# Kernel tuning notes

Hardware: AMD Instinct MI355X
Metric: run time of the kernel (lower is better)

The kernel has to match this reference:

```python
import jax, jax.numpy as jnp
import numpy as np

B, L, D, H, K_DELAYS = 8, 2048, 512, 8, 8
DH = D // H


def setup_inputs() -> dict:
    key = jax.random.key(0)
    ks = jax.random.split(key, 6)
    def lin_w(k):
        return 0.02 * jax.random.normal(k, (D, D), jnp.float32)
    return {
        "x_q":  jax.random.normal(ks[0], (B, L, D), jnp.float32),
        "x_kv": jax.random.normal(ks[1], (B, L, D), jnp.float32),
        "Wq": lin_w(ks[2]), "bq": jnp.zeros((D,), jnp.float32),
        "Wk": lin_w(ks[3]), "bk": jnp.zeros((D,), jnp.float32),
        "Wv": lin_w(ks[4]), "bv": jnp.zeros((D,), jnp.float32),
        "Wo": lin_w(ks[5]), "bo": jnp.zeros((D,), jnp.float32),
    }


def reference(x_q, x_kv, Wq, bq, Wk, bk, Wv, bv, Wo, bo):
    Bx, Lx, Dx = x_q.shape

    def proj(x, W, b):  # torch Linear: x @ W.T + b, then split heads -> [B,H,L,dh]
        return (x @ W.T + b).reshape(Bx, Lx, H, DH).transpose(0, 2, 1, 3)

    q = proj(x_q, Wq, bq)
    k = proj(x_kv, Wk, bk)
    v = proj(x_kv, Wv, bv)

    # FFT-based autocorrelation over the time axis (axis=2)
    qz = q - q.mean(axis=2, keepdims=True)
    kz = k - k.mean(axis=2, keepdims=True)
    Qf = jnp.fft.rfft(qz, axis=2)
    Kf = jnp.fft.rfft(kz, axis=2)
    corr = jnp.fft.irfft(Qf * jnp.conj(Kf), n=Lx, axis=2).mean(axis=-1)  # [B,H,L]
    # torch expands corr to [B,H,Lq,Lk] then means over Lq -> identical to corr
    score = corr

    K = min(K_DELAYS, Lx)
    vals, idx = jax.lax.top_k(score, K)                    # [B,H,K]
    w = vals / (vals.sum(axis=-1, keepdims=True) + 1e-12)
    w = jax.lax.stop_gradient(w)                           # .detach() in torch

    # circular shift by -delay == gather at (t + delay) mod L
    t = jnp.arange(Lx)
    pos = (t[None, None, None, :] + idx[..., None]) % Lx   # [B,H,K,L]
    v_sh = jnp.take_along_axis(v[:, :, None, :, :], pos[..., None], axis=3)  # [B,H,K,L,dh]
    out = jnp.einsum('bhk,bhkld->bhld', w, v_sh)           # weighted sum over delays

    out = out.transpose(0, 2, 1, 3).reshape(Bx, Lx, Dx)
    return out @ Wo.T + bo
```

## Files before the change

### kernel.cpp

```cpp
#include <hip/hip_runtime.h>
#include <math.h>

#define BB 8
#define LL 2048
#define DD 512
#define HH 8
#define DHH 64
#define KD 8
#define MM (BB*LL)

typedef _Float16 f16x2 __attribute__((ext_vector_type(2)));
typedef _Float16 f16x4 __attribute__((ext_vector_type(4)));
typedef _Float16 f16x8 __attribute__((ext_vector_type(8)));
typedef float    f32x4 __attribute__((ext_vector_type(4)));

__device__ inline void cvt8(const float* __restrict__ s, _Float16* hp, _Float16* lp) {
    const float4 a = *(const float4*)s;
    const float4 b = *(const float4*)(s + 4);
    const float v[8] = {a.x, a.y, a.z, a.w, b.x, b.y, b.z, b.w};
    f16x8 hi, lo;
#pragma unroll
    for (int j = 0; j < 8; j++) {
        const _Float16 h = (_Float16)v[j];
        hi[j] = h;
        lo[j] = (_Float16)((v[j] - (float)h) * 512.0f);
    }
    *(f16x8*)hp = hi;
    if (lp) *(f16x8*)lp = lo;
}

__global__ __launch_bounds__(256) void prep_all(const float* __restrict__ xq,
                                                const float* __restrict__ xkv,
                                                const float* __restrict__ Wq, const float* __restrict__ Wk,
                                                const float* __restrict__ Wv, const float* __restrict__ Wo,
                                                _Float16* __restrict__ Xq_h, _Float16* __restrict__ Xq_l,
                                                _Float16* __restrict__ Xkv_h, _Float16* __restrict__ Xkv_l,
                                                _Float16* __restrict__ Wq_h, _Float16* __restrict__ Wq_l,
                                                _Float16* __restrict__ Wk_h, _Float16* __restrict__ Wk_l,
                                                _Float16* __restrict__ Wv_h, _Float16* __restrict__ Wo_h) {
    const int bid = blockIdx.x;
    if (bid < 8192) {
        const int g = bid * 256 + threadIdx.x;
        const int which = g >> 20;
        const size_t idx = (size_t)(g & 1048575) * 8;
        const float* src = which ? xkv : xq;
        _Float16* dh = which ? Xkv_h : Xq_h;
        _Float16* dl = which ? Xkv_l : Xq_l;
        cvt8(src + idx, dh + idx, dl + idx);
    } else {
        const int g = (bid - 8192) * 256 + threadIdx.x;
        const int which = g >> 15;
        const size_t idx = (size_t)(g & 32767) * 8;
        if (which == 0)      cvt8(Wq + idx, Wq_h + idx, Wq_l + idx);
        else if (which == 1) cvt8(Wk + idx, Wk_h + idx, Wk_l + idx);
        else if (which == 2) cvt8(Wv + idx, Wv_h + idx, nullptr);
        else                 cvt8(Wo + idx, Wo_h + idx, nullptr);
    }
}

template<int NPROD, int MODE>
__device__ __forceinline__ void gemm_body(const _Float16* __restrict__ Ag,
                                          const _Float16* __restrict__ Al_g,
                                          const _Float16* __restrict__ Bg,
                                          const _Float16* __restrict__ Bl_g,
                                          const float* __restrict__ bias,
                                          void* __restrict__ Cv,
                                          _Float16* lds, int l0) {
    _Float16* Ah = lds;
    _Float16* Bh = lds + 5120;
    _Float16* Al = (NPROD == 3) ? lds + 10240 : lds;
    _Float16* Bl = (NPROD == 3) ? lds + 15360 : lds;

    const int t  = threadIdx.x;
    const int m0 = (((l0 >> 5) << 3) | (l0 & 7)) * 128;
    const int n0 = ((l0 >> 3) & 3) * 128;

    const int lrow = t >> 2;
    const int lcol = (t & 3) * 8;
    const int wave = t >> 6;
    const int lane = t & 63;
    const int wm   = (wave >> 1) * 64;
    const int wn   = (wave & 1) * 64;
    const int lm   = lane & 15;
    const int quad = lane >> 4;

    f32x4 acc0[4][4] = {};
    f32x4 acc1[4][4] = {};

    f16x8 pa[2], pb[2], pal[2], pbl[2];
#pragma unroll
    for (int p = 0; p < 2; p++) {
        pa[p] = *(const f16x8*)(Ag + (size_t)(m0 + p * 64 + lrow) * 512 + lcol);
        pb[p] = *(const f16x8*)(Bg + (size_t)(n0 + p * 64 + lrow) * 512 + lcol);
        if (NPROD == 3) {
            pal[p] = *(const f16x8*)(Al_g + (size_t)(m0 + p * 64 + lrow) * 512 + lcol);
            pbl[p] = *(const f16x8*)(Bl_g + (size_t)(n0 + p * 64 + lrow) * 512 + lcol);
        }
    }

    for (int k0 = 0; k0 < 512; k0 += 32) {
        __syncthreads();
#pragma unroll
        for (int p = 0; p < 2; p++) {
            const int row = p * 64 + lrow;
            *(f16x8*)&Ah[row * 40 + lcol] = pa[p];
            *(f16x8*)&Bh[row * 40 + lcol] = pb[p];
            if (NPROD == 3) {
                *(f16x8*)&Al[row * 40 + lcol] = pal[p];
                *(f16x8*)&Bl[row * 40 + lcol] = pbl[p];
            }
        }
        __syncthreads();

        if (k0 + 32 < 512) {
            const int kn = k0 + 32;
#pragma unroll
            for (int p = 0; p < 2; p++) {
                pa[p] = *(const f16x8*)(Ag + (size_t)(m0 + p * 64 + lrow) * 512 + kn + lcol);
                pb[p] = *(const f16x8*)(Bg + (size_t)(n0 + p * 64 + lrow) * 512 + kn + lcol);
                if (NPROD == 3) {
                    pal[p] = *(const f16x8*)(Al_g + (size_t)(m0 + p * 64 + lrow) * 512 + kn + lcol);
                    pbl[p] = *(const f16x8*)(Bl_g + (size_t)(n0 + p * 64 + lrow) * 512 + kn + lcol);
                }
            }
        }

        f16x8 afh[4], bf[4];
#pragma unroll
        for (int mt = 0; mt < 4; mt++)
            afh[mt] = *(f16x8*)&Ah[(wm + mt * 16 + lm) * 40 + quad * 8];
#pragma unroll
        for (int nt = 0; nt < 4; nt++)
            bf[nt] = *(f16x8*)&Bh[(wn + nt * 16 + lm) * 40 + quad * 8];

#pragma unroll
        for (int mt = 0; mt < 4; mt++)
#pragma unroll
            for (int nt = 0; nt < 4; nt++)
                acc0[mt][nt] = __builtin_amdgcn_mfma_f32_16x16x32_f16(afh[mt], bf[nt], acc0[mt][nt], 0, 0, 0);

        if (NPROD == 3) {
            f16x8 afl[4];
#pragma unroll
            for (int mt = 0; mt < 4; mt++)
                afl[mt] = *(f16x8*)&Al[(wm + mt * 16 + lm) * 40 + quad * 8];
#pragma unroll
            for (int mt = 0; mt < 4; mt++)
#pragma unroll
                for (int nt = 0; nt < 4; nt++)
                    acc1[mt][nt] = __builtin_amdgcn_mfma_f32_16x16x32_f16(afl[mt], bf[nt], acc1[mt][nt], 0, 0, 0);
#pragma unroll
            for (int nt = 0; nt < 4; nt++)
                bf[nt] = *(f16x8*)&Bl[(wn + nt * 16 + lm) * 40 + quad * 8];
#pragma unroll
            for (int mt = 0; mt < 4; mt++)
#pragma unroll
                for (int nt = 0; nt < 4; nt++)
                    acc1[mt][nt] = __builtin_amdgcn_mfma_f32_16x16x32_f16(afh[mt], bf[nt], acc1[mt][nt], 0, 0, 0);
        }
    }

#pragma unroll
    for (int mt = 0; mt < 4; mt++) {
#pragma unroll
        for (int nt = 0; nt < 4; nt++) {
            const int n = n0 + wn + nt * 16 + lm;
            const float bv = bias[n];
            float val[4];
#pragma unroll
            for (int r = 0; r < 4; r++) {
                val[r] = acc0[mt][nt][r] + bv;
                if (NPROD == 3) val[r] += acc1[mt][nt][r] * (1.0f / 512.0f);
            }
            const int mbase = m0 + wm + mt * 16 + quad * 4;
            const int b_idx = mbase >> 11;
            const int lbase = mbase & 2047;
            if (MODE == 0) {
                float* C = (float*)Cv;
#pragma unroll
                for (int r = 0; r < 4; r++) C[(size_t)(mbase + r) * 512 + n] = val[r];
            } else if (MODE == 1) {
                float* C = (float*)Cv;
                float4 pv = make_float4(val[0], val[1], val[2], val[3]);
                *(float4*)&C[((size_t)(b_idx * 512 + n)) * 2048 + lbase] = pv;
            } else {
                _Float16* C = (_Float16*)Cv;
#pragma unroll
                for (int r = 0; r < 4; r++)
                    C[(size_t)b_idx * 1048576 + (size_t)(n >> 6) * 131072
                      + (size_t)(lbase + r) * 64 + (n & 63)] = (_Float16)val[r];
            }
        }
    }
}

__global__ __launch_bounds__(256, 2) void gemm_qk(const _Float16* __restrict__ A0h, const _Float16* __restrict__ A0l,
                                                  const _Float16* __restrict__ B0h, const _Float16* __restrict__ B0l,
                                                  const float* __restrict__ bias0, float* __restrict__ C0,
                                                  const _Float16* __restrict__ A1h, const _Float16* __restrict__ A1l,
                                                  const _Float16* __restrict__ B1h, const _Float16* __restrict__ B1l,
                                                  const float* __restrict__ bias1, float* __restrict__ C1) {
    __shared__ __align__(16) _Float16 lds[20480];
    const int prob = blockIdx.x >> 9;
    const int l0   = blockIdx.x & 511;
    if (prob == 0)
        gemm_body<3, 1>(A0h, A0l, B0h, B0l, bias0, C0, lds, l0);
    else
        gemm_body<3, 1>(A1h, A1l, B1h, B1l, bias1, C1, lds, l0);
}

__global__ __launch_bounds__(256, 2) void gemm_o(const _Float16* __restrict__ Ah_g,
                                                 const _Float16* __restrict__ Bh_g,
                                                 const float* __restrict__ bias,
                                                 float* __restrict__ C) {
    __shared__ __align__(16) _Float16 lds[10240];
    gemm_body<1, 0>(Ah_g, Ah_g, Bh_g, Bh_g, bias, C, lds, blockIdx.x);
}

#define PAD3(i) ((i) + ((i) >> 3))

__device__ inline float2 cmul2(float2 a, float2 w) {
    return make_float2(a.x * w.x - a.y * w.y, a.x * w.y + a.y * w.x);
}
__device__ inline float2 cadd2(float2 a, float2 b) { return make_float2(a.x + b.x, a.y + b.y); }
__device__ inline float2 csub2(float2 a, float2 b) { return make_float2(a.x - b.x, a.y - b.y); }

__global__ __launch_bounds__(256) void fft_fwd(const float* __restrict__ qT,
                                               const float* __restrict__ kT,
                                               float* __restrict__ specP) {
    const int blk  = blockIdx.x;
    const int bh   = blk >> 4;
    const int part = blk & 15;
    const int t    = threadIdx.x;
    __shared__ float2 Zs[2304];
    __shared__ float2 Wt[1024];

#pragma unroll
    for (int s = 0; s < 4; s++) {
        const int j = t + s * 256;
        float sv, cv;
        __sincosf(2.0f * (float)M_PI * (float)j / 2048.0f, &sv, &cv);
        Wt[j] = make_float2(cv, -sv);
    }

    float2 pacc[8];
#pragma unroll
    for (int s = 0; s < 8; s++) pacc[s] = make_float2(0.0f, 0.0f);

    const int low5 = t & 31, hi3 = t >> 5;
    const int low2 = t & 3,  hi6 = t >> 2;

    for (int j4 = 0; j4 < 4; j4++) {
        const int seq = bh * 64 + part * 4 + j4;
        const float* qp = qT + (size_t)seq * 2048;
        const float* kp = kT + (size_t)seq * 2048;
        float2 z[8];
#pragma unroll
        for (int s = 0; s < 8; s++) z[s] = make_float2(qp[t + 256 * s], kp[t + 256 * s]);
        __syncthreads();

#pragma unroll
        for (int sp = 0; sp < 4; sp++) {
            float2 u = z[sp], v = z[sp + 4];
            z[sp]     = cadd2(u, v);
            z[sp + 4] = cmul2(csub2(u, v), Wt[t + 256 * sp]);
        }
#pragma unroll
        for (int base = 0; base < 8; base += 4)
#pragma unroll
            for (int q2 = 0; q2 < 2; q2++) {
                float2 u = z[base + q2], v = z[base + q2 + 2];
                z[base + q2]     = cadd2(u, v);
                z[base + q2 + 2] = cmul2(csub2(u, v), Wt[2 * (t + 256 * q2)]);
            }
        {
            const float2 w = Wt[4 * t];
#pragma unroll
            for (int e = 0; e < 8; e += 2) {
                float2 u = z[e], v = z[e + 1];
                z[e]     = cadd2(u, v);
                z[e + 1] = cmul2(csub2(u, v), w);
            }
        }

#pragma unroll
        for (int s = 0; s < 8; s++) Zs[PAD3(t + 256 * s)] = z[s];
        __syncthreads();
#pragma unroll
        for (int s = 0; s < 8; s++) z[s] = Zs[PAD3(low5 + 32 * s + 256 * hi3)];

#pragma unroll
        for (int sp = 0; sp < 4; sp++) {
            float2 u = z[sp], v = z[sp + 4];
            z[sp]     = cadd2(u, v);
            z[sp + 4] = cmul2(csub2(u, v), Wt[8 * (low5 + 32 * sp)]);
        }
#pragma unroll
        for (int base = 0; base < 8; base += 4)
#pragma unroll
            for (int q2 = 0; q2 < 2; q2++) {
                float2 u = z[base + q2], v = z[base + q2 + 2];
                z[base + q2]     = cadd2(u, v);
                z[base + q2 + 2] = cmul2(csub2(u, v), Wt[16 * (low5 + 32 * q2)]);
            }
        {
            const float2 w = Wt[32 * low5];
#pragma unroll
            for (int e = 0; e < 8; e += 2) {
                float2 u = z[e], v = z[e + 1];
                z[e]     = cadd2(u, v);
                z[e + 1] = cmul2(csub2(u, v), w);
            }
        }

#pragma unroll
        for (int s = 0; s < 8; s++) Zs[PAD3(low5 + 32 * s + 256 * hi3)] = z[s];
        __syncthreads();
#pragma unroll
        for (int s = 0; s < 8; s++) z[s] = Zs[PAD3(low2 + 4 * s + 32 * hi6)];

#pragma unroll
        for (int sp = 0; sp < 4; sp++) {
            float2 u = z[sp], v = z[sp + 4];
            z[sp]     = cadd2(u, v);
            z[sp + 4] = cmul2(csub2(u, v), Wt[64 * (low2 + 4 * sp)]);
        }
#pragma unroll
        for (int base = 0; base < 8; base += 4)
#pragma unroll
            for (int q2 = 0; q2 < 2; q2++) {
                float2 u = z[base + q2], v = z[base + q2 + 2];
                z[base + q2]     = cadd2(u, v);
                z[base + q2 + 2] = cmul2(csub2(u, v), Wt[128 * (low2 + 4 * q2)]);
            }
        {
            const float2 w = Wt[256 * low2];
#pragma unroll
            for (int e = 0; e < 8; e += 2) {
                float2 u = z[e], v = z[e + 1];
                z[e]     = cadd2(u, v);
                z[e + 1] = cmul2(csub2(u, v), w);
            }
        }

#pragma unroll
        for (int s = 0; s < 8; s++) Zs[PAD3(low2 + 4 * s + 32 * hi6)] = z[s];
        __syncthreads();
#pragma unroll
        for (int s = 0; s < 8; s++) z[s] = Zs[PAD3(8 * t + s)];

#pragma unroll
        for (int base = 0; base < 8; base += 4) {
            {
                float2 u = z[base], v = z[base + 2];
                z[base]     = cadd2(u, v);
                z[base + 2] = csub2(u, v);
            }
            {
                float2 u = z[base + 1], v = z[base + 3];
                float2 d = csub2(u, v);
                z[base + 1] = cadd2(u, v);
                z[base + 3] = make_float2(d.y, -d.x);
            }
        }
#pragma unroll
        for (int e = 0; e < 8; e += 2) {
            float2 u = z[e], v = z[e + 1];
            z[e]     = cadd2(u, v);
            z[e + 1] = csub2(u, v);
        }

#pragma unroll
        for (int s = 0; s < 8; s++) Zs[PAD3(8 * t + s)] = z[s];
        __syncthreads();

#pragma unroll
        for (int s = 0; s < 8; s++) {
            const int p  = t + 256 * s;
            const int f  = (int)(__brev((unsigned)p) >> 21);
            const int fm = (2048 - f) & 2047;
            const int p2 = (int)(__brev((unsigned)fm) >> 21);
            const float2 zf = Zs[PAD3(p)];
            const float2 zm = Zs[PAD3(p2)];
            const float qr = 0.5f * (zf.x + zm.x);
            const float qi = 0.5f * (zf.y - zm.y);
            const float kr = 0.5f * (zf.y + zm.y);
            const float ki = 0.5f * (zm.x - zf.x);
            if (f != 0) {
                pacc[s].x += qr * kr + qi * ki;
                pacc[s].y += qi * kr - qr * ki;
            }
        }
    }

    float2* outp = (float2*)specP + (size_t)blk * 2048;
#pragma unroll
    for (int s = 0; s < 8; s++) outp[t + 256 * s] = pacc[s];
}

__device__ inline void build_twiddle(float2* Wt, int tid, float sign) {
#pragma unroll
    for (int s = 0; s < 4; s++) {
        const int j = tid + s * 256;
        const float a = 2.0f * (float)M_PI * (float)j / 2048.0f;
        float sv, cv;
        __sincosf(a, &sv, &cv);
        Wt[j] = make_float2(cv, sign * sv);
    }
}

__device__ inline void fft2048_stages(float2* Z, const float2* Wt, int tid) {
    for (int st = 0; st < 11; st++) {
        const int half = 1 << st;
        const int shift = 10 - st;
#pragma unroll
        for (int r = 0; r < 4; r++) {
            const int m   = tid + r * 256;
            const int grp = m >> st;
            const int pos = m & (half - 1);
            const int i0  = (grp << (st + 1)) + pos;
            const int i1  = i0 + half;
            const float2 w = Wt[pos << shift];
            const float2 a = Z[i0];
            const float2 b = Z[i1];
            const float tr = b.x * w.x - b.y * w.y;
            const float ti = b.x * w.y + b.y * w.x;
            Z[i0] = make_float2(a.x + tr, a.y + ti);
            Z[i1] = make_float2(a.x - tr, a.y - ti);
        }
        __syncthreads();
    }
}

__global__ __launch_bounds__(256, 2) void gemm_v_fftinv(const _Float16* __restrict__ Ah_g,
                                                        const _Float16* __restrict__ Bh_g,
                                                        const float* __restrict__ bias,
                                                        _Float16* __restrict__ C,
                                                        const float* __restrict__ specP,
                                                        int* __restrict__ delays,
                                                        float* __restrict__ weights) {
    __shared__ __align__(16) char smem[24608];
    const int bid = blockIdx.x;
    const int tid = threadIdx.x;

    if (bid >= 64) {
        gemm_body<1, 2>(Ah_g, Ah_g, Bh_g, Bh_g, bias, C, (_Float16*)smem, bid - 64);
        return;
    }

    const int bh = bid;
    float2* Z  = (float2*)smem;
    float2* Wt = (float2*)(smem + 16384);
    float*  wv = (float*)(smem + 24576);
    int*    wi = (int*)(smem + 24592);

    build_twiddle(Wt, tid, +1.0f);

    const float2* sp = (const float2*)specP + (size_t)bh * 16 * 2048;
#pragma unroll
    for (int s = 0; s < 8; s++) {
        const int p = tid + s * 256;
        float2 acc = make_float2(0.0f, 0.0f);
#pragma unroll
        for (int part = 0; part < 16; part++) {
            const float2 v = sp[part * 2048 + p];
            acc.x += v.x; acc.y += v.y;
        }
        Z[p] = acc;
    }
    __syncthreads();
    fft2048_stages(Z, Wt, tid);

    const float scale = 1.0f / (2048.0f * 64.0f);
    float cv[8];
#pragma unroll
    for (int s = 0; s < 8; s++) cv[s] = Z[tid + s * 256].x * scale;

    float bkv[KD];
    int   bki[KD];
#pragma unroll
    for (int k = 0; k < KD; k++) {
        float lv = -1e30f;
        int   li = 1 << 30;
#pragma unroll
        for (int s = 0; s < 8; s++) {
            const int idx = tid + s * 256;
            if (cv[s] > lv || (cv[s] == lv && idx < li)) { lv = cv[s]; li = idx; }
        }
#pragma unroll
        for (int off = 1; off < 64; off <<= 1) {
            const float v2 = __shfl_xor(lv, off);
            const int   i2 = __shfl_xor(li, off);
            if (v2 > lv || (v2 == lv && i2 < li)) { lv = v2; li = i2; }
        }
        if ((tid & 63) == 0) { wv[tid >> 6] = lv; wi[tid >> 6] = li; }
        __syncthreads();
        float bv = wv[0];
        int   bi = wi[0];
#pragma unroll
        for (int j = 1; j < 4; j++) {
            const float v2 = wv[j];
            const int   i2 = wi[j];
            if (v2 > bv || (v2 == bv && i2 < bi)) { bv = v2; bi = i2; }
        }
        bkv[k] = bv;
        bki[k] = bi;
        if ((bi & 255) == tid) {
            const int slot = bi >> 8;
#pragma unroll
            for (int s = 0; s < 8; s++)
                if (s == slot) cv[s] = -1e30f;
        }
        __syncthreads();
    }

    if (tid == 0) {
        float sum = 0.0f;
#pragma unroll
        for (int k = 0; k < KD; k++) sum += bkv[k];
        const float inv = 1.0f / (sum + 1e-12f);
#pragma unroll
        for (int k = 0; k < KD; k++) {
            weights[bh * KD + k] = bkv[k] * inv;
            delays[bh * KD + k]  = bki[k];
        }
    }
}

__global__ __launch_bounds__(256) void gather_ws(const _Float16* __restrict__ v,
                                                 const int* __restrict__ delays,
                                                 const float* __restrict__ weights,
                                                 _Float16* __restrict__ outb) {
    const int gp = blockIdx.x * 256 + threadIdx.x;
    const int c8 = gp & 63;
    const int m  = gp >> 6;
    const int l  = m & 2047;
    const int b  = m >> 11;
    const int ch = c8 * 8;
    const int h  = ch >> 6;
    const int dh = ch & 63;
    const int bh = b * 8 + h;

    const _Float16* vb = v + (size_t)bh * 131072;
    float a[8] = {};
#pragma unroll
    for (int k = 0; k < KD; k++) {
        const int   d = delays[bh * KD + k];
        const float w = weights[bh * KD + k];
        const int   p = (l + d) & 2047;
        const f16x8 pv = *(const f16x8*)&vb[p * 64 + dh];
#pragma unroll
        for (int j = 0; j < 8; j++) a[j] = fmaf(w, (float)pv[j], a[j]);
    }
    f16x8 ov;
#pragma unroll
    for (int j = 0; j < 8; j++) ov[j] = (_Float16)a[j];
    *(f16x8*)&outb[(size_t)m * 512 + ch] = ov;
}

extern "C" void kernel_launch(void* const* d_in, const int* in_sizes, int n_in,
                              void* d_out, int out_size, void* d_ws, size_t ws_size,
                              hipStream_t stream) {
    const float* x_q  = (const float*)d_in[0];
    const float* x_kv = (const float*)d_in[1];
    const float* Wq   = (const float*)d_in[2];
    const float* bq   = (const float*)d_in[3];
    const float* Wk   = (const float*)d_in[4];
    const float* bk   = (const float*)d_in[5];
    const float* Wv   = (const float*)d_in[6];
    const float* bv   = (const float*)d_in[7];
    const float* Wo   = (const float*)d_in[8];
    const float* bo   = (const float*)d_in[9];
    float* out = (float*)d_out;

    char* ws = (char*)d_ws;
    _Float16* Xq_h  = (_Float16*)(ws + 0);
    _Float16* Xq_l  = (_Float16*)(ws + 16777216);
    _Float16* Xkv_h = (_Float16*)(ws + 33554432);
    _Float16* Xkv_l = (_Float16*)(ws + 50331648);
    _Float16* Wq_h  = (_Float16*)(ws + 67108864);
    _Float16* Wq_l  = (_Float16*)(ws + 67633152);
    _Float16* Wk_h  = (_Float16*)(ws + 68157440);
    _Float16* Wk_l  = (_Float16*)(ws + 68681728);
    _Float16* Wv_h  = (_Float16*)(ws + 69206016);
    _Float16* Wo_h  = (_Float16*)(ws + 69730304);
    int*      dely  = (int*)    (ws + 70254592);
    float*    wgt   = (float*)  (ws + 70256640);
    float*    specP = (float*)  (ws + 50331648);
    _Float16* vh    = (_Float16*)(ws + 0);
    _Float16* gbuf  = (_Float16*)(ws + 16777216);
    float*    qf32  = (float*)d_out;

    dim3 blk(256);

    prep_all<<<dim3(8704), blk, 0, stream>>>(x_q, x_kv, Wq, Wk, Wv, Wo,
                                             Xq_h, Xq_l, Xkv_h, Xkv_l,
                                             Wq_h, Wq_l, Wk_h, Wk_l, Wv_h, Wo_h);

    gemm_qk<<<dim3(512), blk, 0, stream>>>(Xq_h, Xq_l, Wq_h, Wq_l, bq, qf32,
                                           Xq_h, Xq_l, Wq_h, Wq_l, bq, qf32);
    {
        float* kf32_ = (float*)(ws + 0);
        gemm_qk<<<dim3(512), blk, 0, stream>>>(Xkv_h, Xkv_l, Wk_h, Wk_l, bk, kf32_,
                                               Xkv_h, Xkv_l, Wk_h, Wk_l, bk, kf32_);
    }

    fft_fwd<<<dim3(1024), blk, 0, stream>>>(qf32, (float*)(ws + 0), specP);

    gemm_v_fftinv<<<dim3(576), blk, 0, stream>>>(Xkv_h, Wv_h, bv, vh, specP, dely, wgt);

    gather_ws<<<dim3(4096), blk, 0, stream>>>(vh, dely, wgt, gbuf);

    gemm_o<<<dim3(512), blk, 0, stream>>>(gbuf, Wo_h, bo, out);
}
```

Measured before the change: 284.9 us.

## Stage GEMM tiles with direct global-to-LDS loads and merge Q/K projection launches

Replaces the register-prefetch plus LDS-store tile staging in the shared GEMM body with global_load_lds direct copies into an XOR-swizzled, unpadded LDS layout, which shrinks LDS per block. This drops the register round trip, but global latency is no longer hidden behind the previous step's MFMAs. When the workspace is large enough, the Q and K projections also run in one 1024-block launch by placing K in a separate workspace region, removing a launch and its tail.

```diff
diff --git a/kernel.cpp b/kernel.cpp
--- a/kernel.cpp
+++ b/kernel.cpp
@@ -58,6 +58,13 @@
     }
 }
 
+__device__ __forceinline__ void stage16(const _Float16* g, const _Float16* l) {
+    __builtin_amdgcn_global_load_lds(
+        (const __attribute__((address_space(1))) void*)g,
+        (__attribute__((address_space(3))) void*)l,
+        16, 0, 0);
+}
+
 template<int NPROD, int MODE>
 __device__ __forceinline__ void gemm_body(const _Float16* __restrict__ Ag,
                                           const _Float16* __restrict__ Al_g,
@@ -67,71 +74,57 @@
                                           void* __restrict__ Cv,
                                           _Float16* lds, int l0) {
     _Float16* Ah = lds;
-    _Float16* Bh = lds + 5120;
-    _Float16* Al = (NPROD == 3) ? lds + 10240 : lds;
-    _Float16* Bl = (NPROD == 3) ? lds + 15360 : lds;
+    _Float16* Bh = lds + 4096;
+    _Float16* Al = (NPROD == 3) ? lds + 8192  : lds;
+    _Float16* Bl = (NPROD == 3) ? lds + 12288 : lds;
 
     const int t  = threadIdx.x;
     const int m0 = (((l0 >> 5) << 3) | (l0 & 7)) * 128;
     const int n0 = ((l0 >> 3) & 3) * 128;
 
-    const int lrow = t >> 2;
-    const int lcol = (t & 3) * 8;
-    const int wave = t >> 6;
+    const int wv   = t >> 6;
     const int lane = t & 63;
-    const int wm   = (wave >> 1) * 64;
-    const int wn   = (wave & 1) * 64;
+    const int wm   = (wv >> 1) * 64;
+    const int wn   = (wv & 1) * 64;
     const int lm   = lane & 15;
     const int quad = lane >> 4;
 
+    int srow[2], schk[2], sgrp[2];
+#pragma unroll
+    for (int i = 0; i < 2; i++) {
+        const int s = (i * 4 + wv) * 64 + lane;
+        srow[i] = s >> 2;
+        schk[i] = (s & 3) ^ ((srow[i] >> 1) & 3);
+        sgrp[i] = (i * 4 + wv) * 512;
+    }
+
     f32x4 acc0[4][4] = {};
     f32x4 acc1[4][4] = {};
 
-    f16x8 pa[2], pb[2], pal[2], pbl[2];
-#pragma unroll
-    for (int p = 0; p < 2; p++) {
-        pa[p] = *(const f16x8*)(Ag + (size_t)(m0 + p * 64 + lrow) * 512 + lcol);
-        pb[p] = *(const f16x8*)(Bg + (size_t)(n0 + p * 64 + lrow) * 512 + lcol);
-        if (NPROD == 3) {
-            pal[p] = *(const f16x8*)(Al_g + (size_t)(m0 + p * 64 + lrow) * 512 + lcol);
-            pbl[p] = *(const f16x8*)(Bl_g + (size_t)(n0 + p * 64 + lrow) * 512 + lcol);
-        }
-    }
+#define ASWZ(R, q) ((size_t)(R) * 32 + (size_t)((((q) ^ (((R) >> 1) & 3))) * 8))
 
     for (int k0 = 0; k0 < 512; k0 += 32) {
         __syncthreads();
 #pragma unroll
-        for (int p = 0; p < 2; p++) {
-            const int row = p * 64 + lrow;
-            *(f16x8*)&Ah[row * 40 + lcol] = pa[p];
-            *(f16x8*)&Bh[row * 40 + lcol] = pb[p];
+        for (int i = 0; i < 2; i++) {
+            const size_t offA = (size_t)(m0 + srow[i]) * 512 + k0 + schk[i] * 8;
+            const size_t offB = (size_t)(n0 + srow[i]) * 512 + k0 + schk[i] * 8;
+            stage16(Ag + offA, Ah + sgrp[i]);
+            stage16(Bg + offB, Bh + sgrp[i]);
             if (NPROD == 3) {
-                *(f16x8*)&Al[row * 40 + lcol] = pal[p];
-                *(f16x8*)&Bl[row * 40 + lcol] = pbl[p];
-            }
-        }
-        __syncthreads();
-
-        if (k0 + 32 < 512) {
-            const int kn = k0 + 32;
-#pragma unroll
-            for (int p = 0; p < 2; p++) {
-                pa[p] = *(const f16x8*)(Ag + (size_t)(m0 + p * 64 + lrow) * 512 + kn + lcol);
-                pb[p] = *(const f16x8*)(Bg + (size_t)(n0 + p * 64 + lrow) * 512 + kn + lcol);
-                if (NPROD == 3) {
-                    pal[p] = *(const f16x8*)(Al_g + (size_t)(m0 + p * 64 + lrow) * 512 + kn + lcol);
-                    pbl[p] = *(const f16x8*)(Bl_g + (size_t)(n0 + p * 64 + lrow) * 512 + kn + lcol);
-                }
-            }
-        }
+                stage16(Al_g + offA, Al + sgrp[i]);
+                stage16(Bl_g + offB, Bl + sgrp[i]);
+            }
+        }
+        __syncthreads();
 
         f16x8 afh[4], bf[4];
 #pragma unroll
         for (int mt = 0; mt < 4; mt++)
-            afh[mt] = *(f16x8*)&Ah[(wm + mt * 16 + lm) * 40 + quad * 8];
+            afh[mt] = *(f16x8*)&Ah[ASWZ(wm + mt * 16 + lm, quad)];
 #pragma unroll
         for (int nt = 0; nt < 4; nt++)
-            bf[nt] = *(f16x8*)&Bh[(wn + nt * 16 + lm) * 40 + quad * 8];
+            bf[nt] = *(f16x8*)&Bh[ASWZ(wn + nt * 16 + lm, quad)];
 
 #pragma unroll
         for (int mt = 0; mt < 4; mt++)
@@ -143,7 +136,7 @@
             f16x8 afl[4];
 #pragma unroll
             for (int mt = 0; mt < 4; mt++)
-                afl[mt] = *(f16x8*)&Al[(wm + mt * 16 + lm) * 40 + quad * 8];
+                afl[mt] = *(f16x8*)&Al[ASWZ(wm + mt * 16 + lm, quad)];
 #pragma unroll
             for (int mt = 0; mt < 4; mt++)
 #pragma unroll
@@ -151,7 +144,7 @@
                     acc1[mt][nt] = __builtin_amdgcn_mfma_f32_16x16x32_f16(afl[mt], bf[nt], acc1[mt][nt], 0, 0, 0);
 #pragma unroll
             for (int nt = 0; nt < 4; nt++)
-                bf[nt] = *(f16x8*)&Bl[(wn + nt * 16 + lm) * 40 + quad * 8];
+                bf[nt] = *(f16x8*)&Bl[ASWZ(wn + nt * 16 + lm, quad)];
 #pragma unroll
             for (int mt = 0; mt < 4; mt++)
 #pragma unroll
@@ -159,6 +152,7 @@
                     acc1[mt][nt] = __builtin_amdgcn_mfma_f32_16x16x32_f16(afh[mt], bf[nt], acc1[mt][nt], 0, 0, 0);
         }
     }
+#undef ASWZ
 
 #pragma unroll
     for (int mt = 0; mt < 4; mt++) {
@@ -200,7 +194,7 @@
                                                   const _Float16* __restrict__ A1h, const _Float16* __restrict__ A1l,
                                                   const _Float16* __restrict__ B1h, const _Float16* __restrict__ B1l,
                                                   const float* __restrict__ bias1, float* __restrict__ C1) {
-    __shared__ __align__(16) _Float16 lds[20480];
+    __shared__ __align__(16) _Float16 lds[16384];
     const int prob = blockIdx.x >> 9;
     const int l0   = blockIdx.x & 511;
     if (prob == 0)
@@ -213,7 +207,7 @@
                                                  const _Float16* __restrict__ Bh_g,
                                                  const float* __restrict__ bias,
                                                  float* __restrict__ C) {
-    __shared__ __align__(16) _Float16 lds[10240];
+    __shared__ __align__(16) _Float16 lds[8192];
     gemm_body<1, 0>(Ah_g, Ah_g, Bh_g, Bh_g, bias, C, lds, blockIdx.x);
 }
 
@@ -597,15 +591,21 @@
                                              Xq_h, Xq_l, Xkv_h, Xkv_l,
                                              Wq_h, Wq_l, Wk_h, Wk_l, Wv_h, Wo_h);
 
-    gemm_qk<<<dim3(512), blk, 0, stream>>>(Xq_h, Xq_l, Wq_h, Wq_l, bq, qf32,
-                                           Xq_h, Xq_l, Wq_h, Wq_l, bq, qf32);
-    {
-        float* kf32_ = (float*)(ws + 0);
-        gemm_qk<<<dim3(512), blk, 0, stream>>>(Xkv_h, Xkv_l, Wk_h, Wk_l, bk, kf32_,
-                                               Xkv_h, Xkv_l, Wk_h, Wk_l, bk, kf32_);
-    }
-
-    fft_fwd<<<dim3(1024), blk, 0, stream>>>(qf32, (float*)(ws + 0), specP);
+    const size_t kOff  = 70258688;
+    const bool   merged = ws_size >= kOff + 33554432;
+    float* kf32 = merged ? (float*)(ws + kOff) : (float*)(ws + 0);
+
+    if (merged) {
+        gemm_qk<<<dim3(1024), blk, 0, stream>>>(Xq_h, Xq_l, Wq_h, Wq_l, bq, qf32,
+                                                Xkv_h, Xkv_l, Wk_h, Wk_l, bk, kf32);
+    } else {
+        gemm_qk<<<dim3(512), blk, 0, stream>>>(Xq_h, Xq_l, Wq_h, Wq_l, bq, qf32,
+                                               Xq_h, Xq_l, Wq_h, Wq_l, bq, qf32);
+        gemm_qk<<<dim3(512), blk, 0, stream>>>(Xkv_h, Xkv_l, Wk_h, Wk_l, bk, kf32,
+                                               Xkv_h, Xkv_l, Wk_h, Wk_l, bk, kf32);
+    }
+
+    fft_fwd<<<dim3(1024), blk, 0, stream>>>(qf32, kf32, specP);
 
     gemm_v_fftinv<<<dim3(576), blk, 0, stream>>>(Xkv_h, Wv_h, bv, vh, specP, dely, wgt);
 
```

Measured after the change: 277.1 us. -2.7%, faster.
